# Optimization experiments

Measured on AMD Instinct MI355X. Metric: run time of the kernel, lower is better.

## Reference

```python
import jax, jax.numpy as jnp
import numpy as np
import math

S, W, H = 256, 128, 768   # sentence, word, hidden (hidden fixed to 768 by PositionalEncoding)
TOPK = 3                  # len(inputs) > 2 branch: fuse 3 nearest sentences


def positional_encoding(length, d_model):
    # Standard sinusoidal PE, identical to the torch buffer construction.
    pos = jnp.arange(length, dtype=jnp.float32)[:, None]                      # [L,1]
    div = jnp.exp(jnp.arange(0, d_model, 2, dtype=jnp.float32)
                  * (-math.log(10000.0) / d_model))                           # [H/2]
    pe = jnp.zeros((length, d_model), dtype=jnp.float32)
    pe = pe.at[:, 0::2].set(jnp.sin(pos * div))
    pe = pe.at[:, 1::2].set(jnp.cos(pos * div))
    return pe


def setup_inputs() -> dict:
    key = jax.random.key(0)
    inputs = jax.random.normal(key, (S, W, H), dtype=jnp.float32)
    return {"inputs": inputs}


def reference(inputs):
    s, w, h = inputs.shape
    # Pairwise L1 distance between the FIRST word vector of each sentence
    # (matmulCell only ever sees x[i,0,:] and k[0,j,:] == inputs[j,0,:]).
    x0 = inputs[:, 0, :]                                                      # [S,H]
    dist = jnp.sum(jnp.abs(x0[:, None, :] - x0[None, :, :]), axis=-1)         # [S,S]
    # torch.sort ascending -> 3 nearest sentences (self included, dist 0)
    idx = jnp.argsort(dist, axis=1)[:, :TOPK]                                 # [S,3] int
    fused = inputs[idx].reshape(s, TOPK * w, h)                               # [S,3W,H]
    # Positional encoding added to both q/v stream and k stream (same tensor;
    # dropout p=0.1 is identity in eval mode).
    x = fused + positional_encoding(TOPK * w, h)[None]                        # [S,3W,H]
    # Scaled dot-product self-attention per row.
    scores = jnp.einsum('slh,smh->slm', x, x) / jnp.sqrt(jnp.float32(h))      # [S,3W,3W]
    attn = jax.nn.softmax(scores, axis=-1)
    out = jnp.einsum('slm,smh->slh', attn, x)                                 # [S,3W,H]
    # D_Attention keeps only the first word-1 rows of each fused output.
    return out[:, :w - 1, :]                                                  # [S,W-1,H]
```

## Files before the change

kernel.cpp:

```cpp
#include <hip/hip_runtime.h>

#define NS 256
#define NW 128
#define NH 768
#define NL 384
#define WH (NW*NH)
#define OUTROWS 127

typedef __attribute__((ext_vector_type(8))) short short8;
typedef __attribute__((ext_vector_type(8))) unsigned short ushort8;
typedef __attribute__((ext_vector_type(8))) __bf16 bf16x8;
typedef __attribute__((ext_vector_type(4))) float f32x4;

#define XS2_STRIDE 136
#define PS_STRIDE 392
#define SMEM_PS   55296
#define SMEM_RED  (SMEM_PS + 128*PS_STRIDE*2)
#define SMEM_TOTAL (SMEM_RED + 4096)

__device__ __forceinline__ unsigned short bf16b(float f) {
  union { float f; unsigned u; } x; x.f = f;
  return (unsigned short)((x.u + 0x7fffu + ((x.u >> 16) & 1u)) >> 16);
}
__device__ __forceinline__ float b2f(unsigned short h) {
  union { unsigned u; float f; } x; x.u = ((unsigned)h) << 16;
  return x.f;
}
__device__ __forceinline__ unsigned short bfc(float f) {
  __bf16 h = (__bf16)f;
  return __builtin_bit_cast(unsigned short, h);
}

__global__ __launch_bounds__(1024) void k_pre(const float* __restrict__ inp,
                                              int* __restrict__ idxw,
                                              unsigned short* __restrict__ peb,
                                              unsigned short* __restrict__ inpb) {
  const int t = threadIdx.x;
  const int b = blockIdx.x;
  if (b >= 544) {
    size_t base = ((size_t)(b - 544) * 1024 + t) * 8;
    float4 a = *(const float4*)(inp + base);
    float4 c = *(const float4*)(inp + base + 4);
    ushort8 o;
    o[0] = bfc(a.x); o[1] = bfc(a.y); o[2] = bfc(a.z); o[3] = bfc(a.w);
    o[4] = bfc(c.x); o[5] = bfc(c.y); o[6] = bfc(c.z); o[7] = bfc(c.w);
    *(ushort8*)(inpb + base) = o;
    return;
  }
  if (b >= NS) {
    int gid = (b - NS) * 1024 + t;
    int l = gid / NH, d = gid - l * NH;
    const float c = -0.011992630687355995f;
    float dv = __expf((float)(d & ~1) * c);
    float ang = (float)l * dv;
    float v = (d & 1) ? cosf(ang) : sinf(ang);
    peb[gid] = bf16b(v);
    return;
  }
  const int i = b;
  __shared__ float xi[772];
  __shared__ float dist[NS];
  __shared__ unsigned long long wkeys[16];
  for (int h = t; h < NH; h += 1024) xi[h + h / 192] = inp[(size_t)i * WH + h];
  __syncthreads();
  const int c = t >> 2, seg = t & 3;
  const float* __restrict__ row = inp + (size_t)c * WH + seg * 192;
  const float* xis = xi + seg * 193;
  float s = 0.f;
  #pragma unroll 4
  for (int h = 0; h < 192; h += 4) {
    float4 v = *(const float4*)(row + h);
    s += fabsf(xis[h]     - v.x) + fabsf(xis[h + 1] - v.y)
       + fabsf(xis[h + 2] - v.z) + fabsf(xis[h + 3] - v.w);
  }
  s += __shfl_xor(s, 1, 64);
  s += __shfl_xor(s, 2, 64);
  if (seg == 0) dist[c] = s;
  __syncthreads();
  for (int k = 0; k < 3; ++k) {
    float d = (t < NS) ? dist[t] : 3.4e38f;
    unsigned long long key = ((unsigned long long)__float_as_uint(d) << 32) | (unsigned)t;
    #pragma unroll
    for (int dd = 1; dd < 64; dd <<= 1) {
      unsigned long long o = __shfl_xor(key, dd, 64);
      key = (o < key) ? o : key;
    }
    if ((t & 63) == 0) wkeys[t >> 6] = key;
    __syncthreads();
    if (t == 0) {
      unsigned long long best = wkeys[0];
      for (int w = 1; w < 16; ++w) if (wkeys[w] < best) best = wkeys[w];
      int bj = (int)(best & 0xffffffffu);
      idxw[i * 3 + k] = bj;
      dist[bj] = 3.4e38f;
    }
    __syncthreads();
  }
}

__global__ __launch_bounds__(512)
void k_attn(const unsigned short* __restrict__ inpb, const unsigned short* __restrict__ peb,
            const int* __restrict__ idxw, float* __restrict__ out) {
  extern __shared__ char smem[];
  unsigned short* Xs = (unsigned short*)smem;
  unsigned short* Ps = (unsigned short*)(smem + SMEM_PS);
  float* red1 = (float*)(smem + SMEM_RED);
  float* red2 = red1 + 512;

  const int s = blockIdx.x;
  const int tid = threadIdx.x;
  const int lane = tid & 63, wid = tid >> 6;
  const int lrow = lane & 15, lhi = lane >> 4;
  const int i0 = idxw[s * 3 + 0], i1 = idxw[s * 3 + 1], i2 = idxw[s * 3 + 2];

  const f32x4 fz = {0.f, 0.f, 0.f, 0.f};
  f32x4 acc[4][6];
  #pragma unroll
  for (int qs = 0; qs < 4; ++qs)
    #pragma unroll
    for (int kf = 0; kf < 6; ++kf) acc[qs][kf] = fz;

  const int qh = wid & 1, kq = wid >> 1;

  for (int hc = 0; hc < 6; ++hc) {
    const int h0 = hc * 128;
    #pragma unroll
    for (int it = 0; it < 12; ++it) {
      const int src = (it < 4) ? i0 : (it < 8 ? i1 : i2);
      const int rls = (it & 3) * 32 + (tid >> 4);
      const int r   = it * 32 + (tid >> 4);
      const int cc  = (tid & 15) * 8;
      ushort8 xv = *(const ushort8*)&inpb[(size_t)src * WH + (size_t)rls * NH + h0 + cc];
      ushort8 pv = *(const ushort8*)&peb[r * NH + h0 + cc];
      bf16x8 o;
      #pragma unroll
      for (int j = 0; j < 8; ++j) o[j] = (__bf16)(b2f(xv[j]) + b2f(pv[j]));
      *reinterpret_cast<bf16x8*>(&Xs[r * XS2_STRIDE + cc]) = o;
    }
    __syncthreads();
    __builtin_amdgcn_s_setprio(1);
    #pragma unroll
    for (int ks = 0; ks < 128; ks += 32) {
      short8 a[4];
      #pragma unroll
      for (int qs = 0; qs < 4; ++qs)
        a[qs] = *reinterpret_cast<const short8*>(&Xs[(qh * 64 + qs * 16 + lrow) * XS2_STRIDE + ks + lhi * 8]);
      #pragma unroll
      for (int kf = 0; kf < 6; ++kf) {
        short8 b = *reinterpret_cast<const short8*>(&Xs[(kq * 96 + kf * 16 + lrow) * XS2_STRIDE + ks + lhi * 8]);
        #pragma unroll
        for (int qs = 0; qs < 4; ++qs)
          acc[qs][kf] = __builtin_amdgcn_mfma_f32_16x16x32_bf16(a[qs], b, acc[qs][kf], 0, 0, 0);
      }
    }
    __builtin_amdgcn_s_setprio(0);
    __syncthreads();
  }

  const float scale = 0.03608439182435161f;
  float mx[4][4];
  #pragma unroll
  for (int qs = 0; qs < 4; ++qs)
    #pragma unroll
    for (int r = 0; r < 4; ++r) {
      float m = acc[qs][0][r];
      #pragma unroll
      for (int kf = 1; kf < 6; ++kf) m = fmaxf(m, acc[qs][kf][r]);
      #pragma unroll
      for (int d = 1; d < 16; d <<= 1) m = fmaxf(m, __shfl_xor(m, d, 64));
      mx[qs][r] = m;
    }
  if (lrow == 0) {
    #pragma unroll
    for (int qs = 0; qs < 4; ++qs)
      #pragma unroll
      for (int r = 0; r < 4; ++r)
        red1[(qh * 64 + qs * 16 + lhi * 4 + r) * 4 + kq] = mx[qs][r];
  }
  __syncthreads();
  float sm[4][4];
  #pragma unroll
  for (int qs = 0; qs < 4; ++qs)
    #pragma unroll
    for (int r = 0; r < 4; ++r) {
      const int row = qh * 64 + qs * 16 + lhi * 4 + r;
      float4 m0 = *(const float4*)&red1[row * 4];
      mx[qs][r] = fmaxf(fmaxf(m0.x, m0.y), fmaxf(m0.z, m0.w));
      sm[qs][r] = 0.f;
    }
  #pragma unroll
  for (int qs = 0; qs < 4; ++qs)
    #pragma unroll
    for (int kf = 0; kf < 6; ++kf)
      #pragma unroll
      for (int r = 0; r < 4; ++r) {
        float p = __expf((acc[qs][kf][r] - mx[qs][r]) * scale);
        acc[qs][kf][r] = p;
        sm[qs][r] += p;
      }
  #pragma unroll
  for (int qs = 0; qs < 4; ++qs)
    #pragma unroll
    for (int r = 0; r < 4; ++r) {
      #pragma unroll
      for (int d = 1; d < 16; d <<= 1) sm[qs][r] += __shfl_xor(sm[qs][r], d, 64);
    }
  if (lrow == 0) {
    #pragma unroll
    for (int qs = 0; qs < 4; ++qs)
      #pragma unroll
      for (int r = 0; r < 4; ++r)
        red2[(qh * 64 + qs * 16 + lhi * 4 + r) * 4 + kq] = sm[qs][r];
  }
  __syncthreads();
  #pragma unroll
  for (int qs = 0; qs < 4; ++qs)
    #pragma unroll
    for (int r = 0; r < 4; ++r) {
      const int row = qh * 64 + qs * 16 + lhi * 4 + r;
      float4 s0 = *(const float4*)&red2[row * 4];
      sm[qs][r] = 1.0f / ((s0.x + s0.y) + (s0.z + s0.w));
    }
  #pragma unroll
  for (int qs = 0; qs < 4; ++qs)
    #pragma unroll
    for (int kf = 0; kf < 6; ++kf)
      #pragma unroll
      for (int r = 0; r < 4; ++r) {
        const int row = qh * 64 + qs * 16 + lhi * 4 + r;
        const int col = kq * 96 + kf * 16 + lrow;
        *(unsigned short*)((char*)Ps + (((row * PS_STRIDE + col) * 2) ^ (((row >> 3) & 7) << 4))) =
            bfc(acc[qs][kf][r] * sm[qs][r]);
      }
  __syncthreads();

  const int qb = wid & 3, hh = wid >> 2;
  short8 pa[2][12];
  #pragma unroll
  for (int qs = 0; qs < 2; ++qs)
    #pragma unroll
    for (int m0 = 0; m0 < 12; ++m0) {
      const int row = qb * 32 + qs * 16 + lrow;
      pa[qs][m0] = *reinterpret_cast<const short8*>(
          (const char*)Ps + (((row * PS_STRIDE + m0 * 32 + lhi * 8) * 2) ^ (((row >> 3) & 7) << 4)));
    }

  unsigned short* VT = Xs;
  const int rl0 = tid >> 3, c8 = (tid & 7) * 8;
  for (int t4 = 0; t4 < 12; ++t4) {
    const int h0 = t4 * 64;
    #pragma unroll
    for (int it = 0; it < 6; ++it) {
      const int src = (it < 2) ? i0 : (it < 4 ? i1 : i2);
      const int ml = rl0 + (it & 1) * 64;
      const int m  = ml + (it >> 1) * 128;
      ushort8 xv = *(const ushort8*)&inpb[(size_t)src * WH + (size_t)ml * NH + h0 + c8];
      ushort8 pv = *(const ushort8*)&peb[m * NH + h0 + c8];
      #pragma unroll
      for (int j = 0; j < 8; ++j) {
        const int vr = c8 + j;
        VT[((vr * PS_STRIDE) + m) ^ (((vr >> 3) & 7) << 3)] = bfc(b2f(xv[j]) + b2f(pv[j]));
      }
    }
    __syncthreads();
    __builtin_amdgcn_s_setprio(1);
    f32x4 o00 = fz, o01 = fz, o10 = fz, o11 = fz;
    const int vr0 = hh * 32 + lrow, vr1 = vr0 + 16;
    const int sw0 = ((vr0 >> 3) & 7) << 4, sw1 = ((vr1 >> 3) & 7) << 4;
    #pragma unroll
    for (int mm = 0; mm < 12; ++mm) {
      const int moff = (mm * 32 + lhi * 8) * 2;
      short8 b0 = *reinterpret_cast<const short8*>((const char*)VT + ((vr0 * PS_STRIDE * 2 + moff) ^ sw0));
      short8 b1 = *reinterpret_cast<const short8*>((const char*)VT + ((vr1 * PS_STRIDE * 2 + moff) ^ sw1));
      o00 = __builtin_amdgcn_mfma_f32_16x16x32_bf16(pa[0][mm], b0, o00, 0, 0, 0);
      o01 = __builtin_amdgcn_mfma_f32_16x16x32_bf16(pa[0][mm], b1, o01, 0, 0, 0);
      o10 = __builtin_amdgcn_mfma_f32_16x16x32_bf16(pa[1][mm], b0, o10, 0, 0, 0);
      o11 = __builtin_amdgcn_mfma_f32_16x16x32_bf16(pa[1][mm], b1, o11, 0, 0, 0);
    }
    __builtin_amdgcn_s_setprio(0);
    float* ob = out + (size_t)s * (OUTROWS * NH) + h0 + hh * 32 + lrow;
    #pragma unroll
    for (int qs = 0; qs < 2; ++qs)
      #pragma unroll
      for (int hf = 0; hf < 2; ++hf) {
        f32x4 o = (qs == 0) ? (hf == 0 ? o00 : o01) : (hf == 0 ? o10 : o11);
        #pragma unroll
        for (int r = 0; r < 4; ++r) {
          const int q = qb * 32 + qs * 16 + lhi * 4 + r;
          if (q < OUTROWS) ob[(size_t)q * NH + hf * 16] = o[r];
        }
      }
    __syncthreads();
  }
}

extern "C" void kernel_launch(void* const* d_in, const int* in_sizes, int n_in,
                              void* d_out, int out_size, void* d_ws, size_t ws_size,
                              hipStream_t stream) {
  (void)in_sizes; (void)n_in; (void)out_size; (void)ws_size;
  const float* inp = (const float*)d_in[0];
  float* out = (float*)d_out;
  char* ws = (char*)d_ws;

  unsigned short* peb = (unsigned short*)ws;
  int* idxw           = (int*)(ws + 589824);
  unsigned short* inpb= (unsigned short*)(ws + 592896);

  hipLaunchKernelGGL(k_pre, dim3(256 + 288 + 3072), dim3(1024), 0, stream,
                     inp, idxw, peb, inpb);

  hipFuncSetAttribute((const void*)k_attn,
                      hipFuncAttributeMaxDynamicSharedMemorySize, SMEM_TOTAL);
  hipLaunchKernelGGL(k_attn, dim3(256), dim3(512), SMEM_TOTAL, stream,
                     inpb, peb, idxw, out);
}
```

Measured before the change: 127.7 us.

## Split attention per sentence into two query-half blocks with smaller shared tiles

The attention kernel now launches two blocks per sentence, each handling 64 of the 128 needed query rows. K is split across all 8 waves and h-chunks shrink to 64, or 32 for the PV stage, so shared memory drops to about 79KB and more blocks can fit per CU. Cost: each block recomputes the full 384-key X tile and V transpose, doubling global loads of the fused inputs and the QK^T key-side work. It also adds more barrier iterations.

After: 168.3 us. 31.8% more time.

```diff
diff --git a/kernel.cpp b/kernel.cpp
--- a/kernel.cpp
+++ b/kernel.cpp
@@ -12,11 +12,13 @@
 typedef __attribute__((ext_vector_type(8))) __bf16 bf16x8;
 typedef __attribute__((ext_vector_type(4))) float f32x4;
 
-#define XS2_STRIDE 136
+#define XS_STRIDE 72
 #define PS_STRIDE 392
-#define SMEM_PS   55296
-#define SMEM_RED  (SMEM_PS + 128*PS_STRIDE*2)
-#define SMEM_TOTAL (SMEM_RED + 4096)
+#define VT_STRIDE 392
+#define OFF_VT   50176
+#define OFF_RED1 75264
+#define OFF_RED2 77312
+#define SMEM_TOTAL 79360
 
 __device__ __forceinline__ unsigned short bf16b(float f) {
   union { float f; unsigned u; } x; x.f = f;
@@ -103,51 +105,54 @@
             const int* __restrict__ idxw, float* __restrict__ out) {
   extern __shared__ char smem[];
   unsigned short* Xs = (unsigned short*)smem;
-  unsigned short* Ps = (unsigned short*)(smem + SMEM_PS);
-  float* red1 = (float*)(smem + SMEM_RED);
-  float* red2 = red1 + 512;
-
-  const int s = blockIdx.x;
+  unsigned short* Ps = (unsigned short*)smem;
+  unsigned short* VT = (unsigned short*)(smem + OFF_VT);
+  float* red1 = (float*)(smem + OFF_RED1);
+  float* red2 = (float*)(smem + OFF_RED2);
+
+  const int s  = blockIdx.x >> 1;
+  const int qh = blockIdx.x & 1;
   const int tid = threadIdx.x;
   const int lane = tid & 63, wid = tid >> 6;
   const int lrow = lane & 15, lhi = lane >> 4;
   const int i0 = idxw[s * 3 + 0], i1 = idxw[s * 3 + 1], i2 = idxw[s * 3 + 2];
 
   const f32x4 fz = {0.f, 0.f, 0.f, 0.f};
-  f32x4 acc[4][6];
-  #pragma unroll
-  for (int qs = 0; qs < 4; ++qs)
-    #pragma unroll
-    for (int kf = 0; kf < 6; ++kf) acc[qs][kf] = fz;
-
-  const int qh = wid & 1, kq = wid >> 1;
-
-  for (int hc = 0; hc < 6; ++hc) {
-    const int h0 = hc * 128;
-    #pragma unroll
-    for (int it = 0; it < 12; ++it) {
-      const int src = (it < 4) ? i0 : (it < 8 ? i1 : i2);
-      const int rls = (it & 3) * 32 + (tid >> 4);
-      const int r   = it * 32 + (tid >> 4);
-      const int cc  = (tid & 15) * 8;
-      ushort8 xv = *(const ushort8*)&inpb[(size_t)src * WH + (size_t)rls * NH + h0 + cc];
-      ushort8 pv = *(const ushort8*)&peb[r * NH + h0 + cc];
+  f32x4 acc[4][3];
+  #pragma unroll
+  for (int qs = 0; qs < 4; ++qs)
+    #pragma unroll
+    for (int kf = 0; kf < 3; ++kf) acc[qs][kf] = fz;
+
+  const int rl0 = tid >> 3, c8 = (tid & 7) * 8;
+
+  for (int hc = 0; hc < 12; ++hc) {
+    const int h0 = hc * 64;
+    #pragma unroll
+    for (int it = 0; it < 6; ++it) {
+      const int src = (it < 2) ? i0 : (it < 4 ? i1 : i2);
+      const int rl = rl0 + (it & 1) * 64;
+      const int r  = rl + (it >> 1) * 128;
+      ushort8 xv = *(const ushort8*)&inpb[(size_t)src * WH + (size_t)rl * NH + h0 + c8];
+      ushort8 pv = *(const ushort8*)&peb[r * NH + h0 + c8];
       bf16x8 o;
       #pragma unroll
       for (int j = 0; j < 8; ++j) o[j] = (__bf16)(b2f(xv[j]) + b2f(pv[j]));
-      *reinterpret_cast<bf16x8*>(&Xs[r * XS2_STRIDE + cc]) = o;
+      *reinterpret_cast<bf16x8*>(&Xs[r * XS_STRIDE + c8]) = o;
     }
     __syncthreads();
     __builtin_amdgcn_s_setprio(1);
     #pragma unroll
-    for (int ks = 0; ks < 128; ks += 32) {
+    for (int ks = 0; ks < 64; ks += 32) {
       short8 a[4];
       #pragma unroll
       for (int qs = 0; qs < 4; ++qs)
-        a[qs] = *reinterpret_cast<const short8*>(&Xs[(qh * 64 + qs * 16 + lrow) * XS2_STRIDE + ks + lhi * 8]);
-      #pragma unroll
-      for (int kf = 0; kf < 6; ++kf) {
-        short8 b = *reinterpret_cast<const short8*>(&Xs[(kq * 96 + kf * 16 + lrow) * XS2_STRIDE + ks + lhi * 8]);
+        a[qs] = *reinterpret_cast<const short8*>(
+            &Xs[(qh * 64 + qs * 16 + lrow) * XS_STRIDE + ks + lhi * 8]);
+      #pragma unroll
+      for (int kf = 0; kf < 3; ++kf) {
+        short8 b = *reinterpret_cast<const short8*>(
+            &Xs[(wid * 48 + kf * 16 + lrow) * XS_STRIDE + ks + lhi * 8]);
         #pragma unroll
         for (int qs = 0; qs < 4; ++qs)
           acc[qs][kf] = __builtin_amdgcn_mfma_f32_16x16x32_bf16(a[qs], b, acc[qs][kf], 0, 0, 0);
@@ -163,9 +168,7 @@
   for (int qs = 0; qs < 4; ++qs)
     #pragma unroll
     for (int r = 0; r < 4; ++r) {
-      float m = acc[qs][0][r];
-      #pragma unroll
-      for (int kf = 1; kf < 6; ++kf) m = fmaxf(m, acc[qs][kf][r]);
+      float m = fmaxf(fmaxf(acc[qs][0][r], acc[qs][1][r]), acc[qs][2][r]);
       #pragma unroll
       for (int d = 1; d < 16; d <<= 1) m = fmaxf(m, __shfl_xor(m, d, 64));
       mx[qs][r] = m;
@@ -175,7 +178,7 @@
     for (int qs = 0; qs < 4; ++qs)
       #pragma unroll
       for (int r = 0; r < 4; ++r)
-        red1[(qh * 64 + qs * 16 + lhi * 4 + r) * 4 + kq] = mx[qs][r];
+        red1[(qs * 16 + lhi * 4 + r) * 8 + wid] = mx[qs][r];
   }
   __syncthreads();
   float sm[4][4];
@@ -183,15 +186,17 @@
   for (int qs = 0; qs < 4; ++qs)
     #pragma unroll
     for (int r = 0; r < 4; ++r) {
-      const int row = qh * 64 + qs * 16 + lhi * 4 + r;
-      float4 m0 = *(const float4*)&red1[row * 4];
-      mx[qs][r] = fmaxf(fmaxf(m0.x, m0.y), fmaxf(m0.z, m0.w));
+      const int row = qs * 16 + lhi * 4 + r;
+      float4 m0 = *(const float4*)&red1[row * 8];
+      float4 m1 = *(const float4*)&red1[row * 8 + 4];
+      mx[qs][r] = fmaxf(fmaxf(fmaxf(m0.x, m0.y), fmaxf(m0.z, m0.w)),
+                        fmaxf(fmaxf(m1.x, m1.y), fmaxf(m1.z, m1.w)));
       sm[qs][r] = 0.f;
     }
   #pragma unroll
   for (int qs = 0; qs < 4; ++qs)
     #pragma unroll
-    for (int kf = 0; kf < 6; ++kf)
+    for (int kf = 0; kf < 3; ++kf)
       #pragma unroll
       for (int r = 0; r < 4; ++r) {
         float p = __expf((acc[qs][kf][r] - mx[qs][r]) * scale);
@@ -210,86 +215,76 @@
     for (int qs = 0; qs < 4; ++qs)
       #pragma unroll
       for (int r = 0; r < 4; ++r)
-        red2[(qh * 64 + qs * 16 + lhi * 4 + r) * 4 + kq] = sm[qs][r];
-  }
-  __syncthreads();
-  #pragma unroll
-  for (int qs = 0; qs < 4; ++qs)
-    #pragma unroll
-    for (int r = 0; r < 4; ++r) {
-      const int row = qh * 64 + qs * 16 + lhi * 4 + r;
-      float4 s0 = *(const float4*)&red2[row * 4];
-      sm[qs][r] = 1.0f / ((s0.x + s0.y) + (s0.z + s0.w));
-    }
-  #pragma unroll
-  for (int qs = 0; qs < 4; ++qs)
-    #pragma unroll
-    for (int kf = 0; kf < 6; ++kf)
+        red2[(qs * 16 + lhi * 4 + r) * 8 + wid] = sm[qs][r];
+  }
+  __syncthreads();
+  #pragma unroll
+  for (int qs = 0; qs < 4; ++qs)
+    #pragma unroll
+    for (int r = 0; r < 4; ++r) {
+      const int row = qs * 16 + lhi * 4 + r;
+      float4 s0 = *(const float4*)&red2[row * 8];
+      float4 s1 = *(const float4*)&red2[row * 8 + 4];
+      sm[qs][r] = 1.0f / ((s0.x + s0.y) + (s0.z + s0.w) + (s1.x + s1.y) + (s1.z + s1.w));
+    }
+  #pragma unroll
+  for (int qs = 0; qs < 4; ++qs)
+    #pragma unroll
+    for (int kf = 0; kf < 3; ++kf)
       #pragma unroll
       for (int r = 0; r < 4; ++r) {
-        const int row = qh * 64 + qs * 16 + lhi * 4 + r;
-        const int col = kq * 96 + kf * 16 + lrow;
+        const int row = qs * 16 + lhi * 4 + r;
+        const int col = wid * 48 + kf * 16 + lrow;
         *(unsigned short*)((char*)Ps + (((row * PS_STRIDE + col) * 2) ^ (((row >> 3) & 7) << 4))) =
             bfc(acc[qs][kf][r] * sm[qs][r]);
       }
   __syncthreads();
 
-  const int qb = wid & 3, hh = wid >> 2;
-  short8 pa[2][12];
-  #pragma unroll
-  for (int qs = 0; qs < 2; ++qs)
-    #pragma unroll
-    for (int m0 = 0; m0 < 12; ++m0) {
-      const int row = qb * 32 + qs * 16 + lrow;
-      pa[qs][m0] = *reinterpret_cast<const short8*>(
-          (const char*)Ps + (((row * PS_STRIDE + m0 * 32 + lhi * 8) * 2) ^ (((row >> 3) & 7) << 4)));
-    }
-
-  unsigned short* VT = Xs;
-  const int rl0 = tid >> 3, c8 = (tid & 7) * 8;
-  for (int t4 = 0; t4 < 12; ++t4) {
-    const int h0 = t4 * 64;
-    #pragma unroll
-    for (int it = 0; it < 6; ++it) {
-      const int src = (it < 2) ? i0 : (it < 4 ? i1 : i2);
-      const int ml = rl0 + (it & 1) * 64;
-      const int m  = ml + (it >> 1) * 128;
-      ushort8 xv = *(const ushort8*)&inpb[(size_t)src * WH + (size_t)ml * NH + h0 + c8];
-      ushort8 pv = *(const ushort8*)&peb[m * NH + h0 + c8];
+  const int qb = wid & 3, hsub = wid >> 2;
+  short8 pa[12];
+  #pragma unroll
+  for (int m0 = 0; m0 < 12; ++m0) {
+    const int row = qb * 16 + lrow;
+    pa[m0] = *reinterpret_cast<const short8*>(
+        (const char*)Ps + (((row * PS_STRIDE + m0 * 32 + lhi * 8) * 2) ^ (((row >> 3) & 7) << 4)));
+  }
+  const int mB  = (tid >> 2);
+  const int vc8 = (tid & 3) * 8;
+  const int q_out = qh * 64 + qb * 16 + lhi * 4;
+
+  for (int t4 = 0; t4 < 24; ++t4) {
+    const int h0 = t4 * 32;
+    #pragma unroll
+    for (int it = 0; it < 3; ++it) {
+      const int src = (it == 0) ? i0 : (it == 1 ? i1 : i2);
+      const int m = it * 128 + mB;
+      ushort8 xv = *(const ushort8*)&inpb[(size_t)src * WH + (size_t)mB * NH + h0 + vc8];
+      ushort8 pv = *(const ushort8*)&peb[m * NH + h0 + vc8];
       #pragma unroll
       for (int j = 0; j < 8; ++j) {
-        const int vr = c8 + j;
-        VT[((vr * PS_STRIDE) + m) ^ (((vr >> 3) & 7) << 3)] = bfc(b2f(xv[j]) + b2f(pv[j]));
+        const int vr = vc8 + j;
+        VT[((vr * VT_STRIDE) + m) ^ (((vr >> 3) & 3) << 4)] = bfc(b2f(xv[j]) + b2f(pv[j]));
       }
     }
     __syncthreads();
     __builtin_amdgcn_s_setprio(1);
-    f32x4 o00 = fz, o01 = fz, o10 = fz, o11 = fz;
-    const int vr0 = hh * 32 + lrow, vr1 = vr0 + 16;
-    const int sw0 = ((vr0 >> 3) & 7) << 4, sw1 = ((vr1 >> 3) & 7) << 4;
+    f32x4 o = fz;
+    const int vr0 = hsub * 16 + lrow;
+    const int swz = ((vr0 >> 3) & 3) << 5;
     #pragma unroll
     for (int mm = 0; mm < 12; ++mm) {
-      const int moff = (mm * 32 + lhi * 8) * 2;
-      short8 b0 = *reinterpret_cast<const short8*>((const char*)VT + ((vr0 * PS_STRIDE * 2 + moff) ^ sw0));
-      short8 b1 = *reinterpret_cast<const short8*>((const char*)VT + ((vr1 * PS_STRIDE * 2 + moff) ^ sw1));
-      o00 = __builtin_amdgcn_mfma_f32_16x16x32_bf16(pa[0][mm], b0, o00, 0, 0, 0);
-      o01 = __builtin_amdgcn_mfma_f32_16x16x32_bf16(pa[0][mm], b1, o01, 0, 0, 0);
-      o10 = __builtin_amdgcn_mfma_f32_16x16x32_bf16(pa[1][mm], b0, o10, 0, 0, 0);
-      o11 = __builtin_amdgcn_mfma_f32_16x16x32_bf16(pa[1][mm], b1, o11, 0, 0, 0);
+      short8 b = *reinterpret_cast<const short8*>(
+          (const char*)VT + ((vr0 * VT_STRIDE * 2 + (mm * 32 + lhi * 8) * 2) ^ swz));
+      o = __builtin_amdgcn_mfma_f32_16x16x32_bf16(pa[mm], b, o, 0, 0, 0);
     }
     __builtin_amdgcn_s_setprio(0);
-    float* ob = out + (size_t)s * (OUTROWS * NH) + h0 + hh * 32 + lrow;
-    #pragma unroll
-    for (int qs = 0; qs < 2; ++qs)
-      #pragma unroll
-      for (int hf = 0; hf < 2; ++hf) {
-        f32x4 o = (qs == 0) ? (hf == 0 ? o00 : o01) : (hf == 0 ? o10 : o11);
-        #pragma unroll
-        for (int r = 0; r < 4; ++r) {
-          const int q = qb * 32 + qs * 16 + lhi * 4 + r;
-          if (q < OUTROWS) ob[(size_t)q * NH + hf * 16] = o[r];
-        }
-      }
+    const int h = h0 + hsub * 16 + lrow;
+    float* ob = out + (size_t)s * (OUTROWS * NH) + h;
+    #pragma unroll
+    for (int r = 0; r < 4; ++r) {
+      const int q = q_out + r;
+      if (q < OUTROWS) ob[(size_t)q * NH] = o[r];
+    }
     __syncthreads();
   }
 }
@@ -311,6 +306,6 @@
 
   hipFuncSetAttribute((const void*)k_attn,
                       hipFuncAttributeMaxDynamicSharedMemorySize, SMEM_TOTAL);
-  hipLaunchKernelGGL(k_attn, dim3(256), dim3(512), SMEM_TOTAL, stream,
+  hipLaunchKernelGGL(k_attn, dim3(512), dim3(512), SMEM_TOTAL, stream,
                      inpb, peb, idxw, out);
 }
```

## Double attention block to 1024 threads, halving per-wave tiles

Applied to the files above, without the earlier changes.

Raises the attention kernel from 512 to 1024 threads (16 waves) per block. Each wave now covers half as many key columns in the QK^T phase and one 16-row query strip in the PV phase, so accumulators and staging loops shrink. The partial-max/sum reduction is widened to 8 column groups, with an extra barrier so the shared buffer can be reused. The aim is more latency hiding and fewer registers per wave, at the cost of more barrier overhead and less register-level reuse per MFMA.

New measurement: 152.5 us. 1.19x slower.

```diff
diff --git a/kernel.cpp b/kernel.cpp
--- a/kernel.cpp
+++ b/kernel.cpp
@@ -98,14 +98,14 @@
   }
 }
 
-__global__ __launch_bounds__(512)
+__global__ __launch_bounds__(1024) __attribute__((amdgpu_waves_per_eu(4, 4)))
 void k_attn(const unsigned short* __restrict__ inpb, const unsigned short* __restrict__ peb,
             const int* __restrict__ idxw, float* __restrict__ out) {
   extern __shared__ char smem[];
   unsigned short* Xs = (unsigned short*)smem;
+  unsigned short* VT = (unsigned short*)smem;
   unsigned short* Ps = (unsigned short*)(smem + SMEM_PS);
-  float* red1 = (float*)(smem + SMEM_RED);
-  float* red2 = red1 + 512;
+  float* red = (float*)(smem + SMEM_RED);
 
   const int s = blockIdx.x;
   const int tid = threadIdx.x;
@@ -114,23 +114,23 @@
   const int i0 = idxw[s * 3 + 0], i1 = idxw[s * 3 + 1], i2 = idxw[s * 3 + 2];
 
   const f32x4 fz = {0.f, 0.f, 0.f, 0.f};
-  f32x4 acc[4][6];
-  #pragma unroll
-  for (int qs = 0; qs < 4; ++qs)
-    #pragma unroll
-    for (int kf = 0; kf < 6; ++kf) acc[qs][kf] = fz;
+  f32x4 acc[4][3];
+  #pragma unroll
+  for (int qs = 0; qs < 4; ++qs)
+    #pragma unroll
+    for (int kf = 0; kf < 3; ++kf) acc[qs][kf] = fz;
 
   const int qh = wid & 1, kq = wid >> 1;
 
   for (int hc = 0; hc < 6; ++hc) {
     const int h0 = hc * 128;
     #pragma unroll
-    for (int it = 0; it < 12; ++it) {
-      const int src = (it < 4) ? i0 : (it < 8 ? i1 : i2);
-      const int rls = (it & 3) * 32 + (tid >> 4);
-      const int r   = it * 32 + (tid >> 4);
-      const int cc  = (tid & 15) * 8;
-      ushort8 xv = *(const ushort8*)&inpb[(size_t)src * WH + (size_t)rls * NH + h0 + cc];
+    for (int it = 0; it < 6; ++it) {
+      const int src = (it < 2) ? i0 : (it < 4 ? i1 : i2);
+      const int rl = (it & 1) * 64 + (tid >> 4);
+      const int r  = it * 64 + (tid >> 4);
+      const int cc = (tid & 15) * 8;
+      ushort8 xv = *(const ushort8*)&inpb[(size_t)src * WH + (size_t)rl * NH + h0 + cc];
       ushort8 pv = *(const ushort8*)&peb[r * NH + h0 + cc];
       bf16x8 o;
       #pragma unroll
@@ -144,10 +144,12 @@
       short8 a[4];
       #pragma unroll
       for (int qs = 0; qs < 4; ++qs)
-        a[qs] = *reinterpret_cast<const short8*>(&Xs[(qh * 64 + qs * 16 + lrow) * XS2_STRIDE + ks + lhi * 8]);
-      #pragma unroll
-      for (int kf = 0; kf < 6; ++kf) {
-        short8 b = *reinterpret_cast<const short8*>(&Xs[(kq * 96 + kf * 16 + lrow) * XS2_STRIDE + ks + lhi * 8]);
+        a[qs] = *reinterpret_cast<const short8*>(
+            &Xs[(qh * 64 + qs * 16 + lrow) * XS2_STRIDE + ks + lhi * 8]);
+      #pragma unroll
+      for (int kf = 0; kf < 3; ++kf) {
+        short8 b = *reinterpret_cast<const short8*>(
+            &Xs[(kq * 48 + kf * 16 + lrow) * XS2_STRIDE + ks + lhi * 8]);
         #pragma unroll
         for (int qs = 0; qs < 4; ++qs)
           acc[qs][kf] = __builtin_amdgcn_mfma_f32_16x16x32_bf16(a[qs], b, acc[qs][kf], 0, 0, 0);
@@ -163,9 +165,7 @@
   for (int qs = 0; qs < 4; ++qs)
     #pragma unroll
     for (int r = 0; r < 4; ++r) {
-      float m = acc[qs][0][r];
-      #pragma unroll
-      for (int kf = 1; kf < 6; ++kf) m = fmaxf(m, acc[qs][kf][r]);
+      float m = fmaxf(fmaxf(acc[qs][0][r], acc[qs][1][r]), acc[qs][2][r]);
       #pragma unroll
       for (int d = 1; d < 16; d <<= 1) m = fmaxf(m, __shfl_xor(m, d, 64));
       mx[qs][r] = m;
@@ -175,7 +175,7 @@
     for (int qs = 0; qs < 4; ++qs)
       #pragma unroll
       for (int r = 0; r < 4; ++r)
-        red1[(qh * 64 + qs * 16 + lhi * 4 + r) * 4 + kq] = mx[qs][r];
+        red[(qh * 64 + qs * 16 + lhi * 4 + r) * 8 + kq] = mx[qs][r];
   }
   __syncthreads();
   float sm[4][4];
@@ -184,14 +184,16 @@
     #pragma unroll
     for (int r = 0; r < 4; ++r) {
       const int row = qh * 64 + qs * 16 + lhi * 4 + r;
-      float4 m0 = *(const float4*)&red1[row * 4];
-      mx[qs][r] = fmaxf(fmaxf(m0.x, m0.y), fmaxf(m0.z, m0.w));
+      float4 m0 = *(const float4*)&red[row * 8];
+      float4 m1 = *(const float4*)&red[row * 8 + 4];
+      mx[qs][r] = fmaxf(fmaxf(fmaxf(m0.x, m0.y), fmaxf(m0.z, m0.w)),
+                        fmaxf(fmaxf(m1.x, m1.y), fmaxf(m1.z, m1.w)));
       sm[qs][r] = 0.f;
     }
   #pragma unroll
   for (int qs = 0; qs < 4; ++qs)
     #pragma unroll
-    for (int kf = 0; kf < 6; ++kf)
+    for (int kf = 0; kf < 3; ++kf)
       #pragma unroll
       for (int r = 0; r < 4; ++r) {
         float p = __expf((acc[qs][kf][r] - mx[qs][r]) * scale);
@@ -205,12 +207,13 @@
       #pragma unroll
       for (int d = 1; d < 16; d <<= 1) sm[qs][r] += __shfl_xor(sm[qs][r], d, 64);
     }
+  __syncthreads();
   if (lrow == 0) {
     #pragma unroll
     for (int qs = 0; qs < 4; ++qs)
       #pragma unroll
       for (int r = 0; r < 4; ++r)
-        red2[(qh * 64 + qs * 16 + lhi * 4 + r) * 4 + kq] = sm[qs][r];
+        red[(qh * 64 + qs * 16 + lhi * 4 + r) * 8 + kq] = sm[qs][r];
   }
   __syncthreads();
   #pragma unroll
@@ -218,42 +221,40 @@
     #pragma unroll
     for (int r = 0; r < 4; ++r) {
       const int row = qh * 64 + qs * 16 + lhi * 4 + r;
-      float4 s0 = *(const float4*)&red2[row * 4];
-      sm[qs][r] = 1.0f / ((s0.x + s0.y) + (s0.z + s0.w));
-    }
-  #pragma unroll
-  for (int qs = 0; qs < 4; ++qs)
-    #pragma unroll
-    for (int kf = 0; kf < 6; ++kf)
+      float4 s0 = *(const float4*)&red[row * 8];
+      float4 s1 = *(const float4*)&red[row * 8 + 4];
+      sm[qs][r] = 1.0f / ((s0.x + s0.y) + (s0.z + s0.w) + (s1.x + s1.y) + (s1.z + s1.w));
+    }
+  #pragma unroll
+  for (int qs = 0; qs < 4; ++qs)
+    #pragma unroll
+    for (int kf = 0; kf < 3; ++kf)
       #pragma unroll
       for (int r = 0; r < 4; ++r) {
         const int row = qh * 64 + qs * 16 + lhi * 4 + r;
-        const int col = kq * 96 + kf * 16 + lrow;
+        const int col = kq * 48 + kf * 16 + lrow;
         *(unsigned short*)((char*)Ps + (((row * PS_STRIDE + col) * 2) ^ (((row >> 3) & 7) << 4))) =
             bfc(acc[qs][kf][r] * sm[qs][r]);
       }
   __syncthreads();
 
-  const int qb = wid & 3, hh = wid >> 2;
-  short8 pa[2][12];
-  #pragma unroll
-  for (int qs = 0; qs < 2; ++qs)
-    #pragma unroll
-    for (int m0 = 0; m0 < 12; ++m0) {
-      const int row = qb * 32 + qs * 16 + lrow;
-      pa[qs][m0] = *reinterpret_cast<const short8*>(
-          (const char*)Ps + (((row * PS_STRIDE + m0 * 32 + lhi * 8) * 2) ^ (((row >> 3) & 7) << 4)));
-    }
-
-  unsigned short* VT = Xs;
-  const int rl0 = tid >> 3, c8 = (tid & 7) * 8;
+  const int qb = wid & 7, hsub = wid >> 3;
+  short8 pa[12];
+  #pragma unroll
+  for (int m0 = 0; m0 < 12; ++m0) {
+    const int row = qb * 16 + lrow;
+    pa[m0] = *reinterpret_cast<const short8*>(
+        (const char*)Ps + (((row * PS_STRIDE + m0 * 32 + lhi * 8) * 2) ^ (((row >> 3) & 7) << 4)));
+  }
+  const int ml = tid >> 3, c8 = (tid & 7) * 8;
+  const int q_out = qb * 16 + lhi * 4;
+
   for (int t4 = 0; t4 < 12; ++t4) {
     const int h0 = t4 * 64;
     #pragma unroll
-    for (int it = 0; it < 6; ++it) {
-      const int src = (it < 2) ? i0 : (it < 4 ? i1 : i2);
-      const int ml = rl0 + (it & 1) * 64;
-      const int m  = ml + (it >> 1) * 128;
+    for (int it = 0; it < 3; ++it) {
+      const int src = (it == 0) ? i0 : (it == 1 ? i1 : i2);
+      const int m = it * 128 + ml;
       ushort8 xv = *(const ushort8*)&inpb[(size_t)src * WH + (size_t)ml * NH + h0 + c8];
       ushort8 pv = *(const ushort8*)&peb[m * NH + h0 + c8];
       #pragma unroll
@@ -264,32 +265,28 @@
     }
     __syncthreads();
     __builtin_amdgcn_s_setprio(1);
-    f32x4 o00 = fz, o01 = fz, o10 = fz, o11 = fz;
-    const int vr0 = hh * 32 + lrow, vr1 = vr0 + 16;
+    f32x4 o0 = fz, o1 = fz;
+    const int vr0 = hsub * 32 + lrow, vr1 = vr0 + 16;
     const int sw0 = ((vr0 >> 3) & 7) << 4, sw1 = ((vr1 >> 3) & 7) << 4;
     #pragma unroll
     for (int mm = 0; mm < 12; ++mm) {
       const int moff = (mm * 32 + lhi * 8) * 2;
       short8 b0 = *reinterpret_cast<const short8*>((const char*)VT + ((vr0 * PS_STRIDE * 2 + moff) ^ sw0));
       short8 b1 = *reinterpret_cast<const short8*>((const char*)VT + ((vr1 * PS_STRIDE * 2 + moff) ^ sw1));
-      o00 = __builtin_amdgcn_mfma_f32_16x16x32_bf16(pa[0][mm], b0, o00, 0, 0, 0);
-      o01 = __builtin_amdgcn_mfma_f32_16x16x32_bf16(pa[0][mm], b1, o01, 0, 0, 0);
-      o10 = __builtin_amdgcn_mfma_f32_16x16x32_bf16(pa[1][mm], b0, o10, 0, 0, 0);
-      o11 = __builtin_amdgcn_mfma_f32_16x16x32_bf16(pa[1][mm], b1, o11, 0, 0, 0);
+      o0 = __builtin_amdgcn_mfma_f32_16x16x32_bf16(pa[mm], b0, o0, 0, 0, 0);
+      o1 = __builtin_amdgcn_mfma_f32_16x16x32_bf16(pa[mm], b1, o1, 0, 0, 0);
     }
     __builtin_amdgcn_s_setprio(0);
-    float* ob = out + (size_t)s * (OUTROWS * NH) + h0 + hh * 32 + lrow;
-    #pragma unroll
-    for (int qs = 0; qs < 2; ++qs)
-      #pragma unroll
-      for (int hf = 0; hf < 2; ++hf) {
-        f32x4 o = (qs == 0) ? (hf == 0 ? o00 : o01) : (hf == 0 ? o10 : o11);
-        #pragma unroll
-        for (int r = 0; r < 4; ++r) {
-          const int q = qb * 32 + qs * 16 + lhi * 4 + r;
-          if (q < OUTROWS) ob[(size_t)q * NH + hf * 16] = o[r];
-        }
-      }
+    float* ob = out + (size_t)s * (OUTROWS * NH) + h0 + hsub * 32 + lrow;
+    #pragma unroll
+    for (int hf = 0; hf < 2; ++hf) {
+      f32x4 o = hf == 0 ? o0 : o1;
+      #pragma unroll
+      for (int r = 0; r < 4; ++r) {
+        const int q = q_out + r;
+        if (q < OUTROWS) ob[(size_t)q * NH + hf * 16] = o[r];
+      }
+    }
     __syncthreads();
   }
 }
@@ -311,6 +308,6 @@
 
   hipFuncSetAttribute((const void*)k_attn,
                       hipFuncAttributeMaxDynamicSharedMemorySize, SMEM_TOTAL);
-  hipLaunchKernelGGL(k_attn, dim3(256), dim3(512), SMEM_TOTAL, stream,
+  hipLaunchKernelGGL(k_attn, dim3(256), dim3(1024), SMEM_TOTAL, stream,
                      inpb, peb, idxw, out);
 }
```

## Register-prefetch next K/V chunks and use lighter LDS-only barriers

Applied to the files above, without the earlier changes.

Both attention phases now prefetch the next 64-wide hidden chunk of inputs and positional encoding into registers while the current chunk is converted and fed to MFMA. The QK phase shrinks from 128-wide to 64-wide chunks so that prefetch fits in registers. __syncthreads is replaced by an LDS-only waitcnt plus s_barrier, so global loads in flight are not drained at each barrier. The kernel is also pinned to two waves per EU. The aim is to hide global load latency behind compute, at the cost of more registers and twice as many QK barrier rounds.

Measured after the change: 193.0 us. 1.51x slower.

```diff
diff --git a/kernel.cpp b/kernel.cpp
--- a/kernel.cpp
+++ b/kernel.cpp
@@ -12,11 +12,14 @@
 typedef __attribute__((ext_vector_type(8))) __bf16 bf16x8;
 typedef __attribute__((ext_vector_type(4))) float f32x4;
 
-#define XS2_STRIDE 136
+#define XS_STRIDE 72
 #define PS_STRIDE 392
 #define SMEM_PS   55296
 #define SMEM_RED  (SMEM_PS + 128*PS_STRIDE*2)
 #define SMEM_TOTAL (SMEM_RED + 4096)
+
+#define BAR() do { asm volatile("s_waitcnt lgkmcnt(0)" ::: "memory"); \
+                   __builtin_amdgcn_s_barrier(); } while (0)
 
 __device__ __forceinline__ unsigned short bf16b(float f) {
   union { float f; unsigned u; } x; x.f = f;
@@ -98,7 +101,7 @@
   }
 }
 
-__global__ __launch_bounds__(512)
+__global__ __launch_bounds__(512) __attribute__((amdgpu_waves_per_eu(2, 2)))
 void k_attn(const unsigned short* __restrict__ inpb, const unsigned short* __restrict__ peb,
             const int* __restrict__ idxw, float* __restrict__ out) {
   extern __shared__ char smem[];
@@ -121,40 +124,62 @@
     for (int kf = 0; kf < 6; ++kf) acc[qs][kf] = fz;
 
   const int qh = wid & 1, kq = wid >> 1;
-
-  for (int hc = 0; hc < 6; ++hc) {
-    const int h0 = hc * 128;
-    #pragma unroll
-    for (int it = 0; it < 12; ++it) {
-      const int src = (it < 4) ? i0 : (it < 8 ? i1 : i2);
-      const int rls = (it & 3) * 32 + (tid >> 4);
-      const int r   = it * 32 + (tid >> 4);
-      const int cc  = (tid & 15) * 8;
-      ushort8 xv = *(const ushort8*)&inpb[(size_t)src * WH + (size_t)rls * NH + h0 + cc];
-      ushort8 pv = *(const ushort8*)&peb[r * NH + h0 + cc];
+  const int rl0 = tid >> 3, c8 = (tid & 7) * 8;
+
+  ushort8 qx[6], qp[6];
+  #pragma unroll
+  for (int it = 0; it < 6; ++it) {
+    const int src = (it < 2) ? i0 : (it < 4 ? i1 : i2);
+    const int rl = rl0 + (it & 1) * 64;
+    const int r  = rl + (it >> 1) * 128;
+    qx[it] = *(const ushort8*)&inpb[(size_t)src * WH + (size_t)rl * NH + c8];
+    qp[it] = *(const ushort8*)&peb[r * NH + c8];
+  }
+  for (int hc = 0; hc < 12; ++hc) {
+    const int h0 = hc * 64;
+    #pragma unroll
+    for (int it = 0; it < 6; ++it) {
+      const int rl = rl0 + (it & 1) * 64;
+      const int r  = rl + (it >> 1) * 128;
+      ushort8 xv = qx[it], pv = qp[it];
+      if (hc < 11) {
+        const int src = (it < 2) ? i0 : (it < 4 ? i1 : i2);
+        qx[it] = *(const ushort8*)&inpb[(size_t)src * WH + (size_t)rl * NH + h0 + 64 + c8];
+        qp[it] = *(const ushort8*)&peb[r * NH + h0 + 64 + c8];
+      }
       bf16x8 o;
       #pragma unroll
       for (int j = 0; j < 8; ++j) o[j] = (__bf16)(b2f(xv[j]) + b2f(pv[j]));
-      *reinterpret_cast<bf16x8*>(&Xs[r * XS2_STRIDE + cc]) = o;
-    }
-    __syncthreads();
+      *reinterpret_cast<bf16x8*>(&Xs[r * XS_STRIDE + c8]) = o;
+    }
+    BAR();
     __builtin_amdgcn_s_setprio(1);
     #pragma unroll
-    for (int ks = 0; ks < 128; ks += 32) {
+    for (int ks = 0; ks < 64; ks += 32) {
       short8 a[4];
       #pragma unroll
       for (int qs = 0; qs < 4; ++qs)
-        a[qs] = *reinterpret_cast<const short8*>(&Xs[(qh * 64 + qs * 16 + lrow) * XS2_STRIDE + ks + lhi * 8]);
+        a[qs] = *reinterpret_cast<const short8*>(&Xs[(qh * 64 + qs * 16 + lrow) * XS_STRIDE + ks + lhi * 8]);
       #pragma unroll
       for (int kf = 0; kf < 6; ++kf) {
-        short8 b = *reinterpret_cast<const short8*>(&Xs[(kq * 96 + kf * 16 + lrow) * XS2_STRIDE + ks + lhi * 8]);
+        short8 b = *reinterpret_cast<const short8*>(&Xs[(kq * 96 + kf * 16 + lrow) * XS_STRIDE + ks + lhi * 8]);
         #pragma unroll
         for (int qs = 0; qs < 4; ++qs)
           acc[qs][kf] = __builtin_amdgcn_mfma_f32_16x16x32_bf16(a[qs], b, acc[qs][kf], 0, 0, 0);
       }
     }
     __builtin_amdgcn_s_setprio(0);
-    __syncthreads();
+    BAR();
+  }
+
+  ushort8 vx[6], vp[6];
+  #pragma unroll
+  for (int it = 0; it < 6; ++it) {
+    const int src = (it < 2) ? i0 : (it < 4 ? i1 : i2);
+    const int ml = rl0 + (it & 1) * 64;
+    const int m  = ml + (it >> 1) * 128;
+    vx[it] = *(const ushort8*)&inpb[(size_t)src * WH + (size_t)ml * NH + c8];
+    vp[it] = *(const ushort8*)&peb[m * NH + c8];
   }
 
   const float scale = 0.03608439182435161f;
@@ -177,7 +202,7 @@
       for (int r = 0; r < 4; ++r)
         red1[(qh * 64 + qs * 16 + lhi * 4 + r) * 4 + kq] = mx[qs][r];
   }
-  __syncthreads();
+  BAR();
   float sm[4][4];
   #pragma unroll
   for (int qs = 0; qs < 4; ++qs)
@@ -212,7 +237,7 @@
       for (int r = 0; r < 4; ++r)
         red2[(qh * 64 + qs * 16 + lhi * 4 + r) * 4 + kq] = sm[qs][r];
   }
-  __syncthreads();
+  BAR();
   #pragma unroll
   for (int qs = 0; qs < 4; ++qs)
     #pragma unroll
@@ -232,7 +257,7 @@
         *(unsigned short*)((char*)Ps + (((row * PS_STRIDE + col) * 2) ^ (((row >> 3) & 7) << 4))) =
             bfc(acc[qs][kf][r] * sm[qs][r]);
       }
-  __syncthreads();
+  BAR();
 
   const int qb = wid & 3, hh = wid >> 2;
   short8 pa[2][12];
@@ -246,23 +271,25 @@
     }
 
   unsigned short* VT = Xs;
-  const int rl0 = tid >> 3, c8 = (tid & 7) * 8;
   for (int t4 = 0; t4 < 12; ++t4) {
     const int h0 = t4 * 64;
     #pragma unroll
     for (int it = 0; it < 6; ++it) {
-      const int src = (it < 2) ? i0 : (it < 4 ? i1 : i2);
       const int ml = rl0 + (it & 1) * 64;
       const int m  = ml + (it >> 1) * 128;
-      ushort8 xv = *(const ushort8*)&inpb[(size_t)src * WH + (size_t)ml * NH + h0 + c8];
-      ushort8 pv = *(const ushort8*)&peb[m * NH + h0 + c8];
+      ushort8 xv = vx[it], pv = vp[it];
+      if (t4 < 11) {
+        const int src = (it < 2) ? i0 : (it < 4 ? i1 : i2);
+        vx[it] = *(const ushort8*)&inpb[(size_t)src * WH + (size_t)ml * NH + h0 + 64 + c8];
+        vp[it] = *(const ushort8*)&peb[m * NH + h0 + 64 + c8];
+      }
       #pragma unroll
       for (int j = 0; j < 8; ++j) {
         const int vr = c8 + j;
         VT[((vr * PS_STRIDE) + m) ^ (((vr >> 3) & 7) << 3)] = bfc(b2f(xv[j]) + b2f(pv[j]));
       }
     }
-    __syncthreads();
+    BAR();
     __builtin_amdgcn_s_setprio(1);
     f32x4 o00 = fz, o01 = fz, o10 = fz, o11 = fz;
     const int vr0 = hh * 32 + lrow, vr1 = vr0 + 16;
@@ -290,7 +317,7 @@
           if (q < OUTROWS) ob[(size_t)q * NH + hf * 16] = o[r];
         }
       }
-    __syncthreads();
+    BAR();
   }
 }
 
```
